# Performance work log

Hardware: AMD Instinct MI355X
Metric: run time of the kernel (lower is better)

Reference implementation:

```python
import jax, jax.numpy as jnp
import numpy as np

N = 30000      # nodes
E = 480000     # edges per relation (avg degree 16)
H = 4          # GAT heads
D = 64         # out_size per head
F1, F2 = 256, 128   # per-metapath input feature dims
SIN = 256      # sen_in_size
HD = H * D     # 256, semantic-attention in_size
OUT = 64       # final out_size


def _gat(feat, src, dst, W, al, ar, b):
    """DGL GATConv (eval mode, dropout=0), activation=relu6."""
    h = (feat @ W).reshape(N, H, D)                     # [N,H,D]
    el = (h * al).sum(-1)                               # [N,H]
    er = (h * ar).sum(-1)                               # [N,H]
    e = jax.nn.leaky_relu(el[src] + er[dst], 0.2)       # [E,H]
    m = jax.ops.segment_max(e, dst, N)                  # edge-softmax over incoming edges
    p = jnp.exp(e - m[dst])
    s = jax.ops.segment_sum(p, dst, N)
    a = p / s[dst]                                      # [E,H]
    out = jax.ops.segment_sum(a[:, :, None] * h[src], dst, N)  # [N,H,D]
    out = out + b.reshape(1, H, D)
    return jnp.clip(out, 0.0, 6.0).reshape(N, H * D)    # relu6, flatten(1)


def _gcn_layer(x, src, dst, W, b):
    """DGL GraphConv, norm='both': D_in^{-1/2} A D_out^{-1/2} X W (+ b)."""
    ones = jnp.ones(src.shape[0], x.dtype)
    deg_o = jnp.clip(jax.ops.segment_sum(ones, src, N), 1.0, None)
    deg_i = jnp.clip(jax.ops.segment_sum(ones, dst, N), 1.0, None)
    h = (x @ W) * (deg_o[:, None] ** -0.5)
    h = jax.ops.segment_sum(h[src], dst, N) * (deg_i[:, None] ** -0.5)
    return h if b is None else h + b


def setup_inputs():
    key = jax.random.key(0)
    ks = jax.random.split(key, 28)
    f32 = jnp.float32
    nrm = lambda k, shp: jax.random.normal(k, shp, f32) * 0.05
    ri = lambda k, shp: jax.random.randint(k, shp, 0, N, jnp.int32)
    return dict(
        feat0=jax.random.normal(ks[0], (N, F1), f32),
        feat1=jax.random.normal(ks[1], (N, F2), f32),
        sen_feat=jax.random.normal(ks[2], (N, SIN), f32),
        Wgat0=nrm(ks[11], (F1, H * D)), al0=nrm(ks[12], (H, D)), ar0=nrm(ks[13], (H, D)), b0=nrm(ks[14], (H * D,)),
        Wgat1=nrm(ks[15], (F2, H * D)), al1=nrm(ks[16], (H, D)), ar1=nrm(ks[17], (H, D)), b1=nrm(ks[18], (H * D,)),
        Wp1=nrm(ks[19], (HD, OUT)), bp1=nrm(ks[20], (OUT,)), wp2=nrm(ks[21], (OUT,)),
        Wf=nrm(ks[22], (HD, OUT)), bf=nrm(ks[23], (OUT,)),
        Wg1=nrm(ks[24], (SIN, OUT)), bg1=nrm(ks[25], (OUT,)), Wg2=nrm(ks[26], (OUT, OUT)),
        src0=ri(ks[3], (E,)), dst0=ri(ks[4], (E,)),
        src1=ri(ks[5], (E,)), dst1=ri(ks[6], (E,)),
        gsrc=ri(ks[7], (E,)), gdst=ri(ks[8], (E,)),
        asrc=ri(ks[9], (E,)), adst=ri(ks[10], (E,)),
        k=10,
    )


def reference(feat0, feat1, sen_feat,
              Wgat0, al0, ar0, b0, Wgat1, al1, ar1, b1,
              Wp1, bp1, wp2, Wf, bf, Wg1, bg1, Wg2,
              src0, dst0, src1, dst1, gsrc, gdst, asrc, adst, k):
    # per-metapath GAT embeddings
    z0 = _gat(feat0, src0, dst0, Wgat0, al0, ar0, b0)   # [N, HD]
    z1 = _gat(feat1, src1, dst1, Wgat1, al1, ar1, b1)   # [N, HD]
    z = jnp.stack([z0, z1], axis=1)                     # [N, M=2, HD]
    # PathAttention (semantic attention over metapaths)
    w = jnp.tanh(z @ Wp1 + bp1) @ wp2                   # [N, M]
    beta = jax.nn.softmax(w.mean(0))                    # [M]
    fused = jnp.einsum('m,nmf->nf', beta, z)            # [N, HD]
    Femb = fused @ Wf + bf                              # [N, OUT]
    # two-layer GCN on the sentence graph
    p1 = jnp.tanh(_gcn_layer(sen_feat, gsrc, gdst, Wg1, bg1))
    P = _gcn_layer(p1, gsrc, gdst, Wg2, None)           # [N, OUT]
    # spectral loss: fuse embeddings, trace of Laplacian quadratic form on first k dims
    Z = 0.5 * (Femb + P)                                # [N, OUT]
    Zk = Z[:, :k]
    diff = Zk[asrc] - Zk[adst]
    tr = 0.5 * jnp.sum(diff * diff)                     # tr(Zk^T (D - A) Zk)
    return (tr, Z)
```

## Files before the change

kernel.cpp:

```cpp
#include <hip/hip_runtime.h>
#include <math.h>

#define NN 30000
#define NE 480000
#define NBLK 118
#define NMT 235
#define NTRB 7500
#define CAPD 128

typedef unsigned short ushort_t;
typedef unsigned int uint_t;
typedef __attribute__((ext_vector_type(8))) short short8;
typedef __attribute__((ext_vector_type(4))) float f32x4;

__device__ __forceinline__ ushort_t f2bf(float x) {
  uint_t u = __float_as_uint(x);
  u = (u + 0x7FFF + ((u >> 16) & 1)) >> 16;
  return (ushort_t)u;
}
__device__ __forceinline__ float bf2f(ushort_t v) {
  return __uint_as_float(((uint_t)v) << 16);
}

__device__ __forceinline__ float wred(float v) {
#pragma unroll
  for (int off = 32; off > 0; off >>= 1) v += __shfl_xor(v, off);
  return v;
}

__global__ void prep_kernel(float4* __restrict__ zp, const float* __restrict__ W0,
                            const float* __restrict__ W1, const float* __restrict__ W2,
                            const float* __restrict__ W3, const float* __restrict__ W4,
                            ushort_t* __restrict__ T0, ushort_t* __restrict__ T1,
                            ushort_t* __restrict__ T2, ushort_t* __restrict__ T3,
                            ushort_t* __restrict__ T4, const float* __restrict__ F0,
                            const float* __restrict__ F1, ushort_t* __restrict__ B0,
                            ushort_t* __restrict__ B1) {
  int id = blockIdx.x * 256 + threadIdx.x;
  if (id < 52501) {
    zp[id] = make_float4(0.f, 0.f, 0.f, 0.f);
    return;
  }
  int wid = id - 52501;
  if (wid < 147456) {
    const float* W;
    ushort_t* T;
    int K, N, base;
    if (wid < 65536) { W = W0; T = T0; K = 256; N = 256; base = 0; }
    else if (wid < 98304) { W = W1; T = T1; K = 128; N = 256; base = 65536; }
    else if (wid < 114688) { W = W2; T = T2; K = 256; N = 64; base = 98304; }
    else if (wid < 131072) { W = W3; T = T3; K = 256; N = 64; base = 114688; }
    else { W = W4; T = T4; K = 256; N = 64; base = 131072; }
    int l = wid - base;
    int k = l / N, n = l - k * N;
    T[(size_t)n * K + k] = f2bf(W[l]);
    return;
  }
  int cid = wid - 147456;
  const float* S;
  ushort_t* D;
  if (cid < 960000) { S = F0; D = B0; }
  else {
    cid -= 960000;
    if (cid >= 480000) return;
    S = F1; D = B1;
  }
  const float4* p = (const float4*)(S + (size_t)cid * 8);
  float4 a = p[0], b = p[1];
  short8 o;
  o[0] = (short)f2bf(a.x); o[1] = (short)f2bf(a.y);
  o[2] = (short)f2bf(a.z); o[3] = (short)f2bf(a.w);
  o[4] = (short)f2bf(b.x); o[5] = (short)f2bf(b.y);
  o[6] = (short)f2bf(b.z); o[7] = (short)f2bf(b.w);
  *(short8*)(D + (size_t)cid * 8) = o;
}


__device__ __forceinline__ void mfma_core_f32(const float* __restrict__ A0,
                                              const ushort_t* __restrict__ BT, int K, int bm,
                                              short* __restrict__ As, short* __restrict__ Bs,
                                              f32x4 acc[2][4]) {
  int tid = threadIdx.x;
  int lane = tid & 63, w = tid >> 6;
  int q = lane >> 4, mr = lane & 15;
#pragma unroll 1
  for (int k0 = 0; k0 < K; k0 += 32) {
    {
      int r = tid >> 1, hf = tid & 1;
      int gr = bm + r;
      float4 f0 = make_float4(0.f, 0.f, 0.f, 0.f), f1 = f0, f2 = f0, f3 = f0;
      if (gr < NN) {
        const float4* pa = (const float4*)(A0 + (size_t)gr * K + k0 + hf * 16);
        f0 = pa[0]; f1 = pa[1]; f2 = pa[2]; f3 = pa[3];
      }
      short8 lo, hi;
      lo[0] = (short)f2bf(f0.x); lo[1] = (short)f2bf(f0.y);
      lo[2] = (short)f2bf(f0.z); lo[3] = (short)f2bf(f0.w);
      lo[4] = (short)f2bf(f1.x); lo[5] = (short)f2bf(f1.y);
      lo[6] = (short)f2bf(f1.z); lo[7] = (short)f2bf(f1.w);
      hi[0] = (short)f2bf(f2.x); hi[1] = (short)f2bf(f2.y);
      hi[2] = (short)f2bf(f2.z); hi[3] = (short)f2bf(f2.w);
      hi[4] = (short)f2bf(f3.x); hi[5] = (short)f2bf(f3.y);
      hi[6] = (short)f2bf(f3.z); hi[7] = (short)f2bf(f3.w);
      short* dst = As + r * 40 + hf * 16;
      *(short8*)(dst) = lo;
      *(short8*)(dst + 8) = hi;
    }
    {
      int n = tid >> 2, qk = tid & 3;
      short8 bv = *(const short8*)((const short*)BT + (size_t)n * K + k0 + qk * 8);
      *(short8*)(Bs + n * 40 + qk * 8) = bv;
    }
    __syncthreads();
    short8 a0 = *(short8*)(As + (w * 32 + mr) * 40 + q * 8);
    short8 a1 = *(short8*)(As + (w * 32 + 16 + mr) * 40 + q * 8);
#pragma unroll
    for (int j = 0; j < 4; ++j) {
      short8 b = *(short8*)(Bs + (j * 16 + mr) * 40 + q * 8);
      acc[0][j] = __builtin_amdgcn_mfma_f32_16x16x32_bf16(a0, b, acc[0][j], 0, 0, 0);
      acc[1][j] = __builtin_amdgcn_mfma_f32_16x16x32_bf16(a1, b, acc[1][j], 0, 0, 0);
    }
    __syncthreads();
  }
}

__device__ __forceinline__ void mfma_core2_bfK(const ushort_t* __restrict__ A0,
                                               const ushort_t* __restrict__ BT, int K, int bm,
                                               short* __restrict__ As, short* __restrict__ Bs,
                                               f32x4 acc[2][8]) {
  int tid = threadIdx.x;
  int lane = tid & 63, w = tid >> 6;
  int q = lane >> 4, mr = lane & 15;
#pragma unroll 1
  for (int k0 = 0; k0 < K; k0 += 32) {
    {
      int r = tid >> 1, hf = tid & 1;
      int gr = bm + r;
      short8 v0 = {0, 0, 0, 0, 0, 0, 0, 0}, v1 = v0;
      if (gr < NN) {
        const short* p0 = (const short*)A0 + (size_t)gr * K + k0 + hf * 16;
        v0 = *(const short8*)p0;
        v1 = *(const short8*)(p0 + 8);
      }
      short* dst = As + r * 40 + hf * 16;
      *(short8*)(dst) = v0;
      *(short8*)(dst + 8) = v1;
    }
    {
      int n = tid >> 1, qk = tid & 1;
      const short* src = (const short*)BT + (size_t)n * K + k0 + qk * 16;
      short8 b0 = *(const short8*)src;
      short8 b1 = *(const short8*)(src + 8);
      short* d = Bs + n * 40 + qk * 16;
      *(short8*)d = b0;
      *(short8*)(d + 8) = b1;
    }
    __syncthreads();
    short8 a0 = *(short8*)(As + (w * 32 + mr) * 40 + q * 8);
    short8 a1 = *(short8*)(As + (w * 32 + 16 + mr) * 40 + q * 8);
#pragma unroll
    for (int j = 0; j < 8; ++j) {
      short8 b = *(short8*)(Bs + (j * 16 + mr) * 40 + q * 8);
      acc[0][j] = __builtin_amdgcn_mfma_f32_16x16x32_bf16(a0, b, acc[0][j], 0, 0, 0);
      acc[1][j] = __builtin_amdgcn_mfma_f32_16x16x32_bf16(a1, b, acc[1][j], 0, 0, 0);
    }
    __syncthreads();
  }
}

__global__ __launch_bounds__(256) void mfma_all_kernel(
    const ushort_t* __restrict__ fB0, const ushort_t* __restrict__ fB1,
    const float* __restrict__ sen, const ushort_t* __restrict__ WT0,
    const ushort_t* __restrict__ WT1, const ushort_t* __restrict__ Wg1T,
    ushort_t* __restrict__ h0, ushort_t* __restrict__ h1, ushort_t* __restrict__ gcnA,
    const float* __restrict__ al0, const float* __restrict__ ar0, float* __restrict__ el0,
    float* __restrict__ er0, const float* __restrict__ al1, const float* __restrict__ ar1,
    float* __restrict__ el1, float* __restrict__ er1, const float* __restrict__ rdo) {
  __shared__ short As[128 * 40];
  __shared__ short Bs[128 * 40];
  int y = blockIdx.y;
  int bm = blockIdx.x * 128;
  int lane = threadIdx.x & 63, w = threadIdx.x >> 6;
  int q = lane >> 4, mr = lane & 15;
  if (y < 4) {
    int gsel = y >> 1, p = y & 1;
    const ushort_t* A = gsel ? fB1 : fB0;
    int K = gsel ? 128 : 256;
    const ushort_t* WT = gsel ? WT1 : WT0;
    ushort_t* H = gsel ? h1 : h0;
    const float* al = gsel ? al1 : al0;
    const float* ar = gsel ? ar1 : ar0;
    float* el = gsel ? el1 : el0;
    float* er = gsel ? er1 : er0;
    f32x4 acc[2][8];
#pragma unroll
    for (int i = 0; i < 2; ++i)
#pragma unroll
      for (int j = 0; j < 8; ++j) acc[i][j] = (f32x4){0.f, 0.f, 0.f, 0.f};
    mfma_core2_bfK(A, WT + (size_t)p * 128 * K, K, bm, As, Bs, acc);
    float alv[8], arv[8];
#pragma unroll
    for (int j = 0; j < 8; ++j) {
      alv[j] = al[p * 128 + j * 16 + mr];
      arv[j] = ar[p * 128 + j * 16 + mr];
    }
#pragma unroll
    for (int i = 0; i < 2; ++i)
#pragma unroll
      for (int r = 0; r < 4; ++r) {
        int gr = bm + w * 32 + i * 16 + q * 4 + r;
        float pl0 = 0.f, pr0 = 0.f, pl1 = 0.f, pr1 = 0.f;
#pragma unroll
        for (int j = 0; j < 4; ++j) {
          pl0 = fmaf(acc[i][j][r], alv[j], pl0);
          pr0 = fmaf(acc[i][j][r], arv[j], pr0);
          pl1 = fmaf(acc[i][j + 4][r], alv[j + 4], pl1);
          pr1 = fmaf(acc[i][j + 4][r], arv[j + 4], pr1);
        }
#pragma unroll
        for (int m = 1; m < 16; m <<= 1) {
          pl0 += __shfl_xor(pl0, m);
          pr0 += __shfl_xor(pr0, m);
          pl1 += __shfl_xor(pl1, m);
          pr1 += __shfl_xor(pr1, m);
        }
        if (gr < NN) {
          if (mr == 0) {
            el[gr * 4 + 2 * p] = pl0;
            er[gr * 4 + 2 * p] = pr0;
            el[gr * 4 + 2 * p + 1] = pl1;
            er[gr * 4 + 2 * p + 1] = pr1;
          }
#pragma unroll
          for (int j = 0; j < 8; ++j)
            H[(size_t)gr * 256 + p * 128 + j * 16 + mr] = f2bf(acc[i][j][r]);
        }
      }
  } else {
    f32x4 acc[2][4];
#pragma unroll
    for (int i = 0; i < 2; ++i)
#pragma unroll
      for (int j = 0; j < 4; ++j) acc[i][j] = (f32x4){0.f, 0.f, 0.f, 0.f};
    mfma_core_f32(sen, Wg1T, 256, bm, As, Bs, acc);
#pragma unroll
    for (int i = 0; i < 2; ++i)
#pragma unroll
      for (int r = 0; r < 4; ++r) {
        int gr = bm + w * 32 + i * 16 + q * 4 + r;
        if (gr < NN) {
          float sc = rdo[gr];
#pragma unroll
          for (int j = 0; j < 4; ++j)
            gcnA[(size_t)gr * 64 + j * 16 + mr] = f2bf(acc[i][j][r] * sc);
        }
      }
  }
}

__global__ __launch_bounds__(256) void mfma_attnwf_kernel(
    const ushort_t* __restrict__ z0, const ushort_t* __restrict__ z1,
    const ushort_t* __restrict__ WpfT, const float* __restrict__ bp1,
    const float* __restrict__ wp2, float* __restrict__ pbuf, ushort_t* __restrict__ Y0,
    ushort_t* __restrict__ Y1) {
  __shared__ short As[128 * 40];
  __shared__ short Bs[128 * 40];
  __shared__ float wsum[4];
  const ushort_t* A = blockIdx.y ? z1 : z0;
  ushort_t* Y = blockIdx.y ? Y1 : Y0;
  int bm = blockIdx.x * 128;
  f32x4 acc[2][8];
#pragma unroll
  for (int i = 0; i < 2; ++i)
#pragma unroll
    for (int j = 0; j < 8; ++j) acc[i][j] = (f32x4){0.f, 0.f, 0.f, 0.f};
  mfma_core2_bfK(A, WpfT, 256, bm, As, Bs, acc);
  int lane = threadIdx.x & 63, w = threadIdx.x >> 6;
  int q = lane >> 4, mr = lane & 15;
  float local = 0.f;
#pragma unroll
  for (int j = 0; j < 4; ++j) {
    int col = j * 16 + mr;
    float bp = bp1[col], wp = wp2[col];
#pragma unroll
    for (int i = 0; i < 2; ++i)
#pragma unroll
      for (int r = 0; r < 4; ++r) {
        int gr = bm + w * 32 + i * 16 + q * 4 + r;
        if (gr < NN) local += tanhf(acc[i][j][r] + bp) * wp;
      }
  }
  local = wred(local);
  if (lane == 0) wsum[w] = local;
#pragma unroll
  for (int j = 4; j < 8; ++j) {
    int col = (j - 4) * 16 + mr;
#pragma unroll
    for (int i = 0; i < 2; ++i)
#pragma unroll
      for (int r = 0; r < 4; ++r) {
        int gr = bm + w * 32 + i * 16 + q * 4 + r;
        if (gr < NN) Y[(size_t)gr * 64 + col] = f2bf(acc[i][j][r]);
      }
  }
  __syncthreads();
  if (threadIdx.x == 0)
    pbuf[blockIdx.y * NMT + blockIdx.x] = wsum[0] + wsum[1] + wsum[2] + wsum[3];
}

__global__ void hist_kernel(const int* __restrict__ d0, const int* __restrict__ d1,
                            const int* __restrict__ d2, const int* __restrict__ d3,
                            int* __restrict__ cnt) {
  int g = blockIdx.y;
  const int* d = g == 0 ? d0 : g == 1 ? d1 : g == 2 ? d2 : d3;
  int e = blockIdx.x * 256 + threadIdx.x;
  if (e < NE) atomicAdd(&cnt[g * NN + d[e]], 1);
}

__global__ __launch_bounds__(256) void scan_blocks_kernel(const int* __restrict__ cnt,
                                                          int* __restrict__ rows,
                                                          int* __restrict__ bsum) {
  __shared__ int sm[256];
  int g = blockIdx.y, t = threadIdx.x;
  int i = blockIdx.x * 256 + t;
  int v = (i < NN) ? cnt[g * NN + i] : 0;
  sm[t] = v;
  __syncthreads();
#pragma unroll
  for (int off = 1; off < 256; off <<= 1) {
    int tmp = (t >= off) ? sm[t - off] : 0;
    __syncthreads();
    sm[t] += tmp;
    __syncthreads();
  }
  if (i < NN) rows[g * (NN + 1) + i] = sm[t] - v;
  if (t == 255) bsum[g * NBLK + blockIdx.x] = sm[255];
}

__global__ __launch_bounds__(128) void scan_tops_kernel(int* __restrict__ bsum,
                                                        int* __restrict__ boff) {
  __shared__ int sm[128];
  int g = blockIdx.y, t = threadIdx.x;
  int v = (t < NBLK) ? bsum[g * NBLK + t] : 0;
  sm[t] = v;
  __syncthreads();
#pragma unroll
  for (int off = 1; off < 128; off <<= 1) {
    int tmp = (t >= off) ? sm[t - off] : 0;
    __syncthreads();
    sm[t] += tmp;
    __syncthreads();
  }
  if (t < NBLK) boff[g * NBLK + t] = sm[t] - v;
}

__global__ void add_off_kernel(int* __restrict__ rows, const int* __restrict__ boff) {
  int g = blockIdx.y, t = threadIdx.x;
  int i = blockIdx.x * 256 + t;
  if (i < NN) rows[g * (NN + 1) + i] += boff[g * NBLK + blockIdx.x];
  if (blockIdx.x == 0 && t == 0) rows[g * (NN + 1) + NN] = NE;
}

__global__ void scatter_kernel(const int* __restrict__ s0, const int* __restrict__ s1,
                               const int* __restrict__ s2, const int* __restrict__ d0,
                               const int* __restrict__ d1, const int* __restrict__ d2,
                               const int* __restrict__ rows, int* __restrict__ cnt2,
                               int* __restrict__ cols, const int* __restrict__ cnt_deg,
                               float* __restrict__ rdo, float* __restrict__ rdi,
                               const int* __restrict__ rows_g) {
  int g = blockIdx.y;
  if (g == 3) {
    int n = blockIdx.x * 256 + threadIdx.x;
    if (n < NN) {
      rdo[n] = rsqrtf(fmaxf((float)cnt_deg[n], 1.f));
      float di = (float)(rows_g[n + 1] - rows_g[n]);
      rdi[n] = rsqrtf(fmaxf(di, 1.f));
    }
    return;
  }
  const int* sp = g == 0 ? s0 : g == 1 ? s1 : s2;
  const int* dp = g == 0 ? d0 : g == 1 ? d1 : d2;
  int e = blockIdx.x * 256 + threadIdx.x;
  if (e >= NE) return;
  int d = dp[e];
  int pos = rows[g * (NN + 1) + d] + atomicAdd(&cnt2[g * NN + d], 1);
  cols[(size_t)g * NE + pos] = sp[e];
}

__global__ __launch_bounds__(256) void gat_node_kernel(
    const int* __restrict__ rows0, const int* __restrict__ cols0, const float* __restrict__ el0,
    const float* __restrict__ er0, const ushort_t* __restrict__ h0,
    const float* __restrict__ bias0, ushort_t* __restrict__ zz0, const int* __restrict__ rows1,
    const int* __restrict__ cols1, const float* __restrict__ el1, const float* __restrict__ er1,
    const ushort_t* __restrict__ h1, const float* __restrict__ bias1,
    ushort_t* __restrict__ zz1) {
  __shared__ float aw[4][CAPD][4];
  int g = blockIdx.y;
  const int* rows = g ? rows1 : rows0;
  const int* cols = g ? cols1 : cols0;
  const float* el = g ? el1 : el0;
  const float* er = g ? er1 : er0;
  const ushort_t* h = g ? h1 : h0;
  const float* bias = g ? bias1 : bias0;
  ushort_t* z = g ? zz1 : zz0;

  int lane = threadIdx.x & 63, w = threadIdx.x >> 6;
  int n = blockIdx.x * 4 + w;
  int r0 = rows[n], r1 = rows[n + 1];
  int deg = r1 - r0;
  float4 er4 = *(const float4*)&er[n * 4];
  float s0 = 0.f, s1 = 0.f, s2 = 0.f, s3 = 0.f;
  for (int j = lane; j < deg; j += 64) {
    int s = cols[r0 + j];
    float4 elv = *(const float4*)&el[s * 4];
    float v0 = elv.x + er4.x; v0 = v0 > 0.f ? v0 : 0.2f * v0;
    float v1 = elv.y + er4.y; v1 = v1 > 0.f ? v1 : 0.2f * v1;
    float v2 = elv.z + er4.z; v2 = v2 > 0.f ? v2 : 0.2f * v2;
    float v3 = elv.w + er4.w; v3 = v3 > 0.f ? v3 : 0.2f * v3;
    float e0 = __expf(v0), e1 = __expf(v1), e2 = __expf(v2), e3 = __expf(v3);
    s0 += e0; s1 += e1; s2 += e2; s3 += e3;
    if (j < CAPD) {
      aw[w][j][0] = e0; aw[w][j][1] = e1; aw[w][j][2] = e2; aw[w][j][3] = e3;
    }
  }
  s0 = wred(s0); s1 = wred(s1); s2 = wred(s2); s3 = wred(s3);
  __syncthreads();
  int hh = lane >> 4;
  float denom = hh == 0 ? s0 : hh == 1 ? s1 : hh == 2 ? s2 : s3;
  float myer = hh == 0 ? er4.x : hh == 1 ? er4.y : hh == 2 ? er4.z : er4.w;
  float invd = (deg > 0) ? 1.f / denom : 0.f;
  float4 acc = make_float4(0.f, 0.f, 0.f, 0.f);
  int jc = deg < CAPD ? deg : CAPD;
  for (int j = 0; j < jc; j += 16) {
    int si[16];
    float ai[16];
#pragma unroll
    for (int t = 0; t < 16; ++t) {
      int jj = j + t;
      int jx = jj < jc ? jj : jc - 1;
      si[t] = cols[r0 + jx];
      ai[t] = (jj < jc) ? aw[w][jj][hh] : 0.f;
    }
    ushort4 ui[16];
#pragma unroll
    for (int t = 0; t < 16; ++t) ui[t] = *(const ushort4*)&h[(size_t)si[t] * 256 + lane * 4];
#pragma unroll
    for (int t = 0; t < 16; ++t) {
      acc.x = fmaf(ai[t], bf2f(ui[t].x), acc.x);
      acc.y = fmaf(ai[t], bf2f(ui[t].y), acc.y);
      acc.z = fmaf(ai[t], bf2f(ui[t].z), acc.z);
      acc.w = fmaf(ai[t], bf2f(ui[t].w), acc.w);
    }
  }
  for (int j = jc; j < deg; ++j) {
    int s = cols[r0 + j];
    float v = el[s * 4 + hh] + myer;
    v = v > 0.f ? v : 0.2f * v;
    float a = __expf(v);
    ushort4 hu = *(const ushort4*)&h[(size_t)s * 256 + lane * 4];
    acc.x = fmaf(a, bf2f(hu.x), acc.x);
    acc.y = fmaf(a, bf2f(hu.y), acc.y);
    acc.z = fmaf(a, bf2f(hu.z), acc.z);
    acc.w = fmaf(a, bf2f(hu.w), acc.w);
  }
  float4 bv = *(const float4*)&bias[lane * 4];
  ushort4 o;
  o.x = f2bf(fminf(fmaxf(acc.x * invd + bv.x, 0.f), 6.f));
  o.y = f2bf(fminf(fmaxf(acc.y * invd + bv.y, 0.f), 6.f));
  o.z = f2bf(fminf(fmaxf(acc.z * invd + bv.z, 0.f), 6.f));
  o.w = f2bf(fminf(fmaxf(acc.w * invd + bv.w, 0.f), 6.f));
  *(ushort4*)&z[(size_t)n * 256 + lane * 4] = o;
}

__global__ __launch_bounds__(256) void gcn_gather12_kernel(
    const int* __restrict__ rows, const int* __restrict__ cols, const ushort_t* __restrict__ X,
    const float* __restrict__ rdi, const float* __restrict__ bg1, const float* __restrict__ Wg2,
    const float* __restrict__ rdo, ushort_t* __restrict__ out2, const float* __restrict__ pbuf,
    float* __restrict__ wb) {
  __shared__ float psm[4][64];
  int lane = threadIdx.x & 63, w = threadIdx.x >> 6;
  if (blockIdx.x == 0) {
    __shared__ float sm[8];
    int t = threadIdx.x;
    float a0 = 0.f, a1 = 0.f;
    for (int i = t; i < NMT; i += 256) {
      a0 += pbuf[i];
      a1 += pbuf[NMT + i];
    }
    a0 = wred(a0);
    a1 = wred(a1);
    if (lane == 0) { sm[w] = a0; sm[4 + w] = a1; }
    __syncthreads();
    if (t == 0) {
      float w0 = (sm[0] + sm[1] + sm[2] + sm[3]) * (1.0f / NN);
      float w1 = (sm[4] + sm[5] + sm[6] + sm[7]) * (1.0f / NN);
      float mx = fmaxf(w0, w1);
      float e0 = expf(w0 - mx), e1 = expf(w1 - mx);
      float inv = 1.f / (e0 + e1);
      wb[2] = e0 * inv;
      wb[3] = e1 * inv;
    }
  }
  int n = blockIdx.x * 4 + w;
  if (n >= NN) return;
  int r0 = rows[n], r1 = rows[n + 1];
  int eg = lane >> 4, fl = lane & 15;
  float facc[4] = {0.f, 0.f, 0.f, 0.f};
  for (int j = r0; j < r1; j += 16) {
    int si[4];
    float sel[4];
#pragma unroll
    for (int t = 0; t < 4; ++t) {
      int jj = j + 4 * t + eg;
      int jx = jj < r1 ? jj : r1 - 1;
      si[t] = cols[jx];
      sel[t] = (jj < r1) ? 1.f : 0.f;
    }
    ushort4 xv[4];
#pragma unroll
    for (int t = 0; t < 4; ++t) xv[t] = *(const ushort4*)&X[(size_t)si[t] * 64 + fl * 4];
#pragma unroll
    for (int t = 0; t < 4; ++t) {
      facc[0] = fmaf(sel[t], bf2f(xv[t].x), facc[0]);
      facc[1] = fmaf(sel[t], bf2f(xv[t].y), facc[1]);
      facc[2] = fmaf(sel[t], bf2f(xv[t].z), facc[2]);
      facc[3] = fmaf(sel[t], bf2f(xv[t].w), facc[3]);
    }
  }
#pragma unroll
  for (int u = 0; u < 4; ++u) {
    facc[u] += __shfl_xor(facc[u], 16);
    facc[u] += __shfl_xor(facc[u], 32);
  }
  if (eg == 0) *(float4*)&psm[w][fl * 4] = make_float4(facc[0], facc[1], facc[2], facc[3]);
  __syncthreads();
  float p = tanhf(psm[w][lane] * rdi[n] + bg1[lane]);
  float o = 0.f;
#pragma unroll
  for (int k = 0; k < 64; ++k) o = fmaf(__shfl(p, k), Wg2[k * 64 + lane], o);
  out2[(size_t)n * 64 + lane] = f2bf(o * rdo[n]);
}

__global__ __launch_bounds__(256) void gcn_gather2_kernel(
    const int* __restrict__ rows, const int* __restrict__ cols, const ushort_t* __restrict__ X,
    const float* __restrict__ rdi, const ushort_t* __restrict__ Y0,
    const ushort_t* __restrict__ Y1, const float* __restrict__ wb, const float* __restrict__ bf,
    const int* __restrict__ kptr, float* __restrict__ Zc, float* __restrict__ dout) {
  int lane = threadIdx.x & 63, w = threadIdx.x >> 6;
  int n = blockIdx.x * 4 + w;
  if (n >= NN) return;
  int r0 = rows[n], r1 = rows[n + 1];
  int eg = lane >> 4, fl = lane & 15;
  float facc[4] = {0.f, 0.f, 0.f, 0.f};
  for (int j = r0; j < r1; j += 16) {
    int si[4];
    float sel[4];
#pragma unroll
    for (int t = 0; t < 4; ++t) {
      int jj = j + 4 * t + eg;
      int jx = jj < r1 ? jj : r1 - 1;
      si[t] = cols[jx];
      sel[t] = (jj < r1) ? 1.f : 0.f;
    }
    ushort4 xv[4];
#pragma unroll
    for (int t = 0; t < 4; ++t) xv[t] = *(const ushort4*)&X[(size_t)si[t] * 64 + fl * 4];
#pragma unroll
    for (int t = 0; t < 4; ++t) {
      facc[0] = fmaf(sel[t], bf2f(xv[t].x), facc[0]);
      facc[1] = fmaf(sel[t], bf2f(xv[t].y), facc[1]);
      facc[2] = fmaf(sel[t], bf2f(xv[t].z), facc[2]);
      facc[3] = fmaf(sel[t], bf2f(xv[t].w), facc[3]);
    }
  }
#pragma unroll
  for (int u = 0; u < 4; ++u) {
    facc[u] += __shfl_xor(facc[u], 16);
    facc[u] += __shfl_xor(facc[u], 32);
  }
  if (eg == 0) {
    float ri = rdi[n];
    ushort4 y0 = *(const ushort4*)&Y0[(size_t)n * 64 + fl * 4];
    ushort4 y1 = *(const ushort4*)&Y1[(size_t)n * 64 + fl * 4];
    float4 bfv = *(const float4*)&bf[fl * 4];
    float w2 = wb[2], w3 = wb[3];
    float zv[4];
    zv[0] = 0.5f * (w2 * bf2f(y0.x) + w3 * bf2f(y1.x) + bfv.x + facc[0] * ri);
    zv[1] = 0.5f * (w2 * bf2f(y0.y) + w3 * bf2f(y1.y) + bfv.y + facc[1] * ri);
    zv[2] = 0.5f * (w2 * bf2f(y0.z) + w3 * bf2f(y1.z) + bfv.z + facc[2] * ri);
    zv[3] = 0.5f * (w2 * bf2f(y0.w) + w3 * bf2f(y1.w) + bfv.w + facc[3] * ri);
    float* dp = dout + 1 + (size_t)n * 64 + fl * 4;
    dp[0] = zv[0]; dp[1] = zv[1]; dp[2] = zv[2]; dp[3] = zv[3];
    int k = *kptr;
    if (fl < 4) {
      float4 zk;
      zk.x = (fl * 4 + 0 < k) ? zv[0] : 0.f;
      zk.y = (fl * 4 + 1 < k) ? zv[1] : 0.f;
      zk.z = (fl * 4 + 2 < k) ? zv[2] : 0.f;
      zk.w = (fl * 4 + 3 < k) ? zv[3] : 0.f;
      *(float4*)&Zc[(size_t)n * 16 + fl * 4] = zk;
    }
  }
}

__global__ __launch_bounds__(256) void tr_kernel(const int* __restrict__ asrc,
                                                 const int* __restrict__ adst,
                                                 const int* __restrict__ kptr,
                                                 const float* __restrict__ Zc,
                                                 const float* __restrict__ dout,
                                                 float* __restrict__ trbuf) {
  __shared__ float wsum[4];
  int lane = threadIdx.x & 63, w = threadIdx.x >> 6;
  int k = *kptr;
  int eg = lane >> 2, c0 = (lane & 3) * 4;
  int e = blockIdx.x * 64 + w * 16 + eg;
  float local = 0.f;
  if (e < NE) {
    int a = asrc[e], b = adst[e];
    if (k <= 16) {
      float4 za = *(const float4*)&Zc[(size_t)a * 16 + c0];
      float4 zb = *(const float4*)&Zc[(size_t)b * 16 + c0];
      float dx = za.x - zb.x, dy = za.y - zb.y, dz = za.z - zb.z, dw = za.w - zb.w;
      local = dx * dx + dy * dy + dz * dz + dw * dw;
    } else {
      const float* Za = dout + 1 + (size_t)a * 64;
      const float* Zb = dout + 1 + (size_t)b * 64;
#pragma unroll
      for (int st = 0; st < 4; ++st) {
#pragma unroll
        for (int t = 0; t < 4; ++t) {
          int c = c0 + st * 16 + t;
          if (c < k) {
            float d2 = Za[c] - Zb[c];
            local += d2 * d2;
          }
        }
      }
    }
  }
#pragma unroll
  for (int off = 32; off > 0; off >>= 1) local += __shfl_down(local, off);
  if (lane == 0) wsum[w] = local;
  __syncthreads();
  if (threadIdx.x == 0) trbuf[blockIdx.x] = wsum[0] + wsum[1] + wsum[2] + wsum[3];
}

__global__ __launch_bounds__(256) void tr_reduce_kernel(const float* __restrict__ trbuf,
                                                        float* __restrict__ dout) {
  __shared__ float sm[4];
  int t = threadIdx.x;
  float a = 0.f;
  for (int i = t; i < NTRB; i += 256) a += trbuf[i];
  a = wred(a);
  int lane = t & 63, w = t >> 6;
  if (lane == 0) sm[w] = a;
  __syncthreads();
  if (t == 0) dout[0] = 0.5f * (sm[0] + sm[1] + sm[2] + sm[3]);
}

extern "C" void kernel_launch(void* const* d_in, const int* in_sizes, int n_in, void* d_out,
                              int out_size, void* d_ws, size_t ws_size, hipStream_t stream) {
  const float* feat0 = (const float*)d_in[0];
  const float* feat1 = (const float*)d_in[1];
  const float* sen = (const float*)d_in[2];
  const float* Wgat0 = (const float*)d_in[3];
  const float* al0 = (const float*)d_in[4];
  const float* ar0 = (const float*)d_in[5];
  const float* b0 = (const float*)d_in[6];
  const float* Wgat1 = (const float*)d_in[7];
  const float* al1 = (const float*)d_in[8];
  const float* ar1 = (const float*)d_in[9];
  const float* b1 = (const float*)d_in[10];
  const float* Wp1 = (const float*)d_in[11];
  const float* bp1 = (const float*)d_in[12];
  const float* wp2 = (const float*)d_in[13];
  const float* Wf = (const float*)d_in[14];
  const float* bf = (const float*)d_in[15];
  const float* Wg1 = (const float*)d_in[16];
  const float* bg1 = (const float*)d_in[17];
  const float* Wg2 = (const float*)d_in[18];
  const int* src0 = (const int*)d_in[19];
  const int* dst0 = (const int*)d_in[20];
  const int* src1 = (const int*)d_in[21];
  const int* dst1 = (const int*)d_in[22];
  const int* gsrc = (const int*)d_in[23];
  const int* gdst = (const int*)d_in[24];
  const int* asrc = (const int*)d_in[25];
  const int* adst = (const int*)d_in[26];
  const int* kptr = (const int*)d_in[27];
  float* out = (float*)d_out;
  float* ws = (float*)d_ws;

  float* wb = ws;
  int* cnt = (int*)(ws + 4);
  int* cnt2 = (int*)(ws + 120004);
  float* rdo = ws + 210004;
  float* rdi = ws + 240004;
  int* rows = (int*)(ws + 270004);
  int* bsum = (int*)(ws + 360008);
  int* boff = (int*)(ws + 360364);
  int* cols = (int*)(ws + 360720);
  float* el0 = ws + 1800720;
  float* er0 = ws + 1920720;
  float* el1 = ws + 2040720;
  float* er1 = ws + 2160720;
  float* pbuf = ws + 2280720;
  float* trbuf = el0;
  ushort_t* h0 = (ushort_t*)(ws + 2283068);
  ushort_t* h1 = (ushort_t*)(ws + 6123068);
  ushort_t* z0 = (ushort_t*)(ws + 9963068);
  ushort_t* z1 = (ushort_t*)(ws + 13803068);
  ushort_t* gcnA = (ushort_t*)(ws + 17643068);
  ushort_t* gcnA2 = (ushort_t*)(ws + 18603068);
  ushort_t* Y0 = (ushort_t*)(ws + 19563068);
  ushort_t* Y1 = (ushort_t*)(ws + 20523068);
  ushort_t* WT0 = (ushort_t*)(ws + 21483068);
  ushort_t* WT1 = (ushort_t*)(ws + 21515836);
  ushort_t* WpfT = (ushort_t*)(ws + 21532220);
  ushort_t* Wg1T = (ushort_t*)(ws + 21548604);
  float* Zc = ws + 21556796;

  int* rows_g = rows + 2 * (NN + 1);
  int* cols_g = cols + 2 * NE;
  int* cnt_deg = cnt + 3 * NN;

  ushort_t* fB0 = z0;
  ushort_t* fB1 = z1;

  prep_kernel<<<6407, 256, 0, stream>>>((float4*)ws, Wgat0, Wgat1, Wp1, Wf, Wg1, WT0, WT1, WpfT,
                                        WpfT + 16384, Wg1T, feat0, feat1, fB0, fB1);

  hist_kernel<<<dim3(1875, 4), 256, 0, stream>>>(dst0, dst1, gdst, gsrc, cnt);
  scan_blocks_kernel<<<dim3(NBLK, 3), 256, 0, stream>>>(cnt, rows, bsum);
  scan_tops_kernel<<<dim3(1, 3), 128, 0, stream>>>(bsum, boff);
  add_off_kernel<<<dim3(NBLK, 3), 256, 0, stream>>>(rows, boff);
  scatter_kernel<<<dim3(1875, 4), 256, 0, stream>>>(src0, src1, gsrc, dst0, dst1, gdst, rows,
                                                    cnt2, cols, cnt_deg, rdo, rdi, rows_g);

  mfma_all_kernel<<<dim3(NMT, 5), 256, 0, stream>>>(fB0, fB1, sen, WT0, WT1, Wg1T, h0, h1,
                                                    gcnA, al0, ar0, el0, er0, al1, ar1, el1,
                                                    er1, rdo);

  gat_node_kernel<<<dim3(7500, 2), 256, 0, stream>>>(rows, cols, el0, er0, h0, b0, z0,
                                                     rows + (NN + 1), cols + NE, el1, er1, h1,
                                                     b1, z1);

  mfma_attnwf_kernel<<<dim3(NMT, 2), 256, 0, stream>>>(z0, z1, WpfT, bp1, wp2, pbuf, Y0, Y1);

  gcn_gather12_kernel<<<7500, 256, 0, stream>>>(rows_g, cols_g, gcnA, rdi, bg1, Wg2, rdo, gcnA2,
                                                pbuf, wb);
  gcn_gather2_kernel<<<7500, 256, 0, stream>>>(rows_g, cols_g, gcnA2, rdi, Y0, Y1, wb, bf, kptr,
                                               Zc, out);

  tr_kernel<<<NTRB, 256, 0, stream>>>(asrc, adst, kptr, Zc, out, trbuf);
  tr_reduce_kernel<<<1, 256, 0, stream>>>(trbuf, out);
}
```

Baseline: 515.7 us.

## Merge GAT aggregation and first GCN gather into one launch; inline beta softmax

The GAT node aggregation for both metapaths and the first GCN gather-plus-Wg2 layer become one kernel launch with 22500 blocks. Block index ranges pick which branch runs, so the independent GCN work can fill the GPU alongside the GAT gathers. The semantic-attention softmax that used to be done by block 0 of the GCN kernel and written to wb is now recomputed per wave inside gcn_gather2 from pbuf. This removes a launch and a global round-trip, at the cost of every wave re-reducing 2x235 partial sums.

```diff
diff --git a/kernel.cpp b/kernel.cpp
--- a/kernel.cpp
+++ b/kernel.cpp
@@ -387,120 +387,158 @@
   cols[(size_t)g * NE + pos] = sp[e];
 }
 
-__global__ __launch_bounds__(256) void gat_node_kernel(
+__global__ __launch_bounds__(256) void gat_g12_kernel(
     const int* __restrict__ rows0, const int* __restrict__ cols0, const float* __restrict__ el0,
     const float* __restrict__ er0, const ushort_t* __restrict__ h0,
     const float* __restrict__ bias0, ushort_t* __restrict__ zz0, const int* __restrict__ rows1,
     const int* __restrict__ cols1, const float* __restrict__ el1, const float* __restrict__ er1,
     const ushort_t* __restrict__ h1, const float* __restrict__ bias1,
-    ushort_t* __restrict__ zz1) {
+    ushort_t* __restrict__ zz1, const int* __restrict__ rows_g, const int* __restrict__ cols_g,
+    const ushort_t* __restrict__ X, const float* __restrict__ rdi,
+    const float* __restrict__ bg1, const float* __restrict__ Wg2,
+    const float* __restrict__ rdo, ushort_t* __restrict__ out2) {
   __shared__ float aw[4][CAPD][4];
-  int g = blockIdx.y;
-  const int* rows = g ? rows1 : rows0;
-  const int* cols = g ? cols1 : cols0;
-  const float* el = g ? el1 : el0;
-  const float* er = g ? er1 : er0;
-  const ushort_t* h = g ? h1 : h0;
-  const float* bias = g ? bias1 : bias0;
-  ushort_t* z = g ? zz1 : zz0;
-
   int lane = threadIdx.x & 63, w = threadIdx.x >> 6;
-  int n = blockIdx.x * 4 + w;
-  int r0 = rows[n], r1 = rows[n + 1];
-  int deg = r1 - r0;
-  float4 er4 = *(const float4*)&er[n * 4];
-  float s0 = 0.f, s1 = 0.f, s2 = 0.f, s3 = 0.f;
-  for (int j = lane; j < deg; j += 64) {
-    int s = cols[r0 + j];
-    float4 elv = *(const float4*)&el[s * 4];
-    float v0 = elv.x + er4.x; v0 = v0 > 0.f ? v0 : 0.2f * v0;
-    float v1 = elv.y + er4.y; v1 = v1 > 0.f ? v1 : 0.2f * v1;
-    float v2 = elv.z + er4.z; v2 = v2 > 0.f ? v2 : 0.2f * v2;
-    float v3 = elv.w + er4.w; v3 = v3 > 0.f ? v3 : 0.2f * v3;
-    float e0 = __expf(v0), e1 = __expf(v1), e2 = __expf(v2), e3 = __expf(v3);
-    s0 += e0; s1 += e1; s2 += e2; s3 += e3;
-    if (j < CAPD) {
-      aw[w][j][0] = e0; aw[w][j][1] = e1; aw[w][j][2] = e2; aw[w][j][3] = e3;
-    }
-  }
-  s0 = wred(s0); s1 = wred(s1); s2 = wred(s2); s3 = wred(s3);
-  __syncthreads();
-  int hh = lane >> 4;
-  float denom = hh == 0 ? s0 : hh == 1 ? s1 : hh == 2 ? s2 : s3;
-  float myer = hh == 0 ? er4.x : hh == 1 ? er4.y : hh == 2 ? er4.z : er4.w;
-  float invd = (deg > 0) ? 1.f / denom : 0.f;
-  float4 acc = make_float4(0.f, 0.f, 0.f, 0.f);
-  int jc = deg < CAPD ? deg : CAPD;
-  for (int j = 0; j < jc; j += 16) {
-    int si[16];
-    float ai[16];
-#pragma unroll
-    for (int t = 0; t < 16; ++t) {
-      int jj = j + t;
-      int jx = jj < jc ? jj : jc - 1;
-      si[t] = cols[r0 + jx];
-      ai[t] = (jj < jc) ? aw[w][jj][hh] : 0.f;
-    }
-    ushort4 ui[16];
-#pragma unroll
-    for (int t = 0; t < 16; ++t) ui[t] = *(const ushort4*)&h[(size_t)si[t] * 256 + lane * 4];
-#pragma unroll
-    for (int t = 0; t < 16; ++t) {
-      acc.x = fmaf(ai[t], bf2f(ui[t].x), acc.x);
-      acc.y = fmaf(ai[t], bf2f(ui[t].y), acc.y);
-      acc.z = fmaf(ai[t], bf2f(ui[t].z), acc.z);
-      acc.w = fmaf(ai[t], bf2f(ui[t].w), acc.w);
-    }
-  }
-  for (int j = jc; j < deg; ++j) {
-    int s = cols[r0 + j];
-    float v = el[s * 4 + hh] + myer;
-    v = v > 0.f ? v : 0.2f * v;
-    float a = __expf(v);
-    ushort4 hu = *(const ushort4*)&h[(size_t)s * 256 + lane * 4];
-    acc.x = fmaf(a, bf2f(hu.x), acc.x);
-    acc.y = fmaf(a, bf2f(hu.y), acc.y);
-    acc.z = fmaf(a, bf2f(hu.z), acc.z);
-    acc.w = fmaf(a, bf2f(hu.w), acc.w);
-  }
-  float4 bv = *(const float4*)&bias[lane * 4];
-  ushort4 o;
-  o.x = f2bf(fminf(fmaxf(acc.x * invd + bv.x, 0.f), 6.f));
-  o.y = f2bf(fminf(fmaxf(acc.y * invd + bv.y, 0.f), 6.f));
-  o.z = f2bf(fminf(fmaxf(acc.z * invd + bv.z, 0.f), 6.f));
-  o.w = f2bf(fminf(fmaxf(acc.w * invd + bv.w, 0.f), 6.f));
-  *(ushort4*)&z[(size_t)n * 256 + lane * 4] = o;
-}
-
-__global__ __launch_bounds__(256) void gcn_gather12_kernel(
+  int bx = blockIdx.x;
+  if (bx < 15000) {
+    int g = bx >= 7500;
+    int bl = g ? bx - 7500 : bx;
+    const int* rows = g ? rows1 : rows0;
+    const int* cols = g ? cols1 : cols0;
+    const float* el = g ? el1 : el0;
+    const float* er = g ? er1 : er0;
+    const ushort_t* h = g ? h1 : h0;
+    const float* bias = g ? bias1 : bias0;
+    ushort_t* z = g ? zz1 : zz0;
+
+    int n = bl * 4 + w;
+    int r0 = rows[n], r1 = rows[n + 1];
+    int deg = r1 - r0;
+    float4 er4 = *(const float4*)&er[n * 4];
+    float s0 = 0.f, s1 = 0.f, s2 = 0.f, s3 = 0.f;
+    for (int j = lane; j < deg; j += 64) {
+      int s = cols[r0 + j];
+      float4 elv = *(const float4*)&el[s * 4];
+      float v0 = elv.x + er4.x; v0 = v0 > 0.f ? v0 : 0.2f * v0;
+      float v1 = elv.y + er4.y; v1 = v1 > 0.f ? v1 : 0.2f * v1;
+      float v2 = elv.z + er4.z; v2 = v2 > 0.f ? v2 : 0.2f * v2;
+      float v3 = elv.w + er4.w; v3 = v3 > 0.f ? v3 : 0.2f * v3;
+      float e0 = __expf(v0), e1 = __expf(v1), e2 = __expf(v2), e3 = __expf(v3);
+      s0 += e0; s1 += e1; s2 += e2; s3 += e3;
+      if (j < CAPD) {
+        aw[w][j][0] = e0; aw[w][j][1] = e1; aw[w][j][2] = e2; aw[w][j][3] = e3;
+      }
+    }
+    s0 = wred(s0); s1 = wred(s1); s2 = wred(s2); s3 = wred(s3);
+    __syncthreads();
+    int hh = lane >> 4;
+    float denom = hh == 0 ? s0 : hh == 1 ? s1 : hh == 2 ? s2 : s3;
+    float myer = hh == 0 ? er4.x : hh == 1 ? er4.y : hh == 2 ? er4.z : er4.w;
+    float invd = (deg > 0) ? 1.f / denom : 0.f;
+    float4 acc = make_float4(0.f, 0.f, 0.f, 0.f);
+    int jc = deg < CAPD ? deg : CAPD;
+    for (int j = 0; j < jc; j += 16) {
+      int si[16];
+      float ai[16];
+#pragma unroll
+      for (int t = 0; t < 16; ++t) {
+        int jj = j + t;
+        int jx = jj < jc ? jj : jc - 1;
+        si[t] = cols[r0 + jx];
+        ai[t] = (jj < jc) ? aw[w][jj][hh] : 0.f;
+      }
+      ushort4 ui[16];
+#pragma unroll
+      for (int t = 0; t < 16; ++t) ui[t] = *(const ushort4*)&h[(size_t)si[t] * 256 + lane * 4];
+#pragma unroll
+      for (int t = 0; t < 16; ++t) {
+        acc.x = fmaf(ai[t], bf2f(ui[t].x), acc.x);
+        acc.y = fmaf(ai[t], bf2f(ui[t].y), acc.y);
+        acc.z = fmaf(ai[t], bf2f(ui[t].z), acc.z);
+        acc.w = fmaf(ai[t], bf2f(ui[t].w), acc.w);
+      }
+    }
+    for (int j = jc; j < deg; ++j) {
+      int s = cols[r0 + j];
+      float v = el[s * 4 + hh] + myer;
+      v = v > 0.f ? v : 0.2f * v;
+      float a = __expf(v);
+      ushort4 hu = *(const ushort4*)&h[(size_t)s * 256 + lane * 4];
+      acc.x = fmaf(a, bf2f(hu.x), acc.x);
+      acc.y = fmaf(a, bf2f(hu.y), acc.y);
+      acc.z = fmaf(a, bf2f(hu.z), acc.z);
+      acc.w = fmaf(a, bf2f(hu.w), acc.w);
+    }
+    float4 bv = *(const float4*)&bias[lane * 4];
+    ushort4 o;
+    o.x = f2bf(fminf(fmaxf(acc.x * invd + bv.x, 0.f), 6.f));
+    o.y = f2bf(fminf(fmaxf(acc.y * invd + bv.y, 0.f), 6.f));
+    o.z = f2bf(fminf(fmaxf(acc.z * invd + bv.z, 0.f), 6.f));
+    o.w = f2bf(fminf(fmaxf(acc.w * invd + bv.w, 0.f), 6.f));
+    *(ushort4*)&z[(size_t)n * 256 + lane * 4] = o;
+  } else {
+    float(*psm)[64] = (float(*)[64])aw;
+    int n = (bx - 15000) * 4 + w;
+    if (n >= NN) return;
+    int r0 = rows_g[n], r1 = rows_g[n + 1];
+    int eg = lane >> 4, fl = lane & 15;
+    float facc[4] = {0.f, 0.f, 0.f, 0.f};
+    for (int j = r0; j < r1; j += 16) {
+      int si[4];
+      float sel[4];
+#pragma unroll
+      for (int t = 0; t < 4; ++t) {
+        int jj = j + 4 * t + eg;
+        int jx = jj < r1 ? jj : r1 - 1;
+        si[t] = cols_g[jx];
+        sel[t] = (jj < r1) ? 1.f : 0.f;
+      }
+      ushort4 xv[4];
+#pragma unroll
+      for (int t = 0; t < 4; ++t) xv[t] = *(const ushort4*)&X[(size_t)si[t] * 64 + fl * 4];
+#pragma unroll
+      for (int t = 0; t < 4; ++t) {
+        facc[0] = fmaf(sel[t], bf2f(xv[t].x), facc[0]);
+        facc[1] = fmaf(sel[t], bf2f(xv[t].y), facc[1]);
+        facc[2] = fmaf(sel[t], bf2f(xv[t].z), facc[2]);
+        facc[3] = fmaf(sel[t], bf2f(xv[t].w), facc[3]);
+      }
+    }
+#pragma unroll
+    for (int u = 0; u < 4; ++u) {
+      facc[u] += __shfl_xor(facc[u], 16);
+      facc[u] += __shfl_xor(facc[u], 32);
+    }
+    if (eg == 0) *(float4*)&psm[w][fl * 4] = make_float4(facc[0], facc[1], facc[2], facc[3]);
+    __syncthreads();
+    float p = tanhf(psm[w][lane] * rdi[n] + bg1[lane]);
+    float o = 0.f;
+#pragma unroll
+    for (int k = 0; k < 64; ++k) o = fmaf(__shfl(p, k), Wg2[k * 64 + lane], o);
+    out2[(size_t)n * 64 + lane] = f2bf(o * rdo[n]);
+  }
+}
+
+__global__ __launch_bounds__(256) void gcn_gather2_kernel(
     const int* __restrict__ rows, const int* __restrict__ cols, const ushort_t* __restrict__ X,
-    const float* __restrict__ rdi, const float* __restrict__ bg1, const float* __restrict__ Wg2,
-    const float* __restrict__ rdo, ushort_t* __restrict__ out2, const float* __restrict__ pbuf,
-    float* __restrict__ wb) {
-  __shared__ float psm[4][64];
+    const float* __restrict__ rdi, const ushort_t* __restrict__ Y0,
+    const ushort_t* __restrict__ Y1, const float* __restrict__ pbuf,
+    const float* __restrict__ bf, const int* __restrict__ kptr, float* __restrict__ Zc,
+    float* __restrict__ dout) {
   int lane = threadIdx.x & 63, w = threadIdx.x >> 6;
-  if (blockIdx.x == 0) {
-    __shared__ float sm[8];
-    int t = threadIdx.x;
-    float a0 = 0.f, a1 = 0.f;
-    for (int i = t; i < NMT; i += 256) {
-      a0 += pbuf[i];
-      a1 += pbuf[NMT + i];
-    }
-    a0 = wred(a0);
-    a1 = wred(a1);
-    if (lane == 0) { sm[w] = a0; sm[4 + w] = a1; }
-    __syncthreads();
-    if (t == 0) {
-      float w0 = (sm[0] + sm[1] + sm[2] + sm[3]) * (1.0f / NN);
-      float w1 = (sm[4] + sm[5] + sm[6] + sm[7]) * (1.0f / NN);
-      float mx = fmaxf(w0, w1);
-      float e0 = expf(w0 - mx), e1 = expf(w1 - mx);
-      float inv = 1.f / (e0 + e1);
-      wb[2] = e0 * inv;
-      wb[3] = e1 * inv;
-    }
-  }
+  float b0a = 0.f, b1a = 0.f;
+  for (int i = lane; i < NMT; i += 64) {
+    b0a += pbuf[i];
+    b1a += pbuf[NMT + i];
+  }
+  b0a = wred(b0a);
+  b1a = wred(b1a);
+  float w0 = b0a * (1.0f / NN), w1 = b1a * (1.0f / NN);
+  float mx = fmaxf(w0, w1);
+  float be0 = __expf(w0 - mx), be1 = __expf(w1 - mx);
+  float binv = 1.f / (be0 + be1);
+  float wb2 = be0 * binv, wb3 = be1 * binv;
+
   int n = blockIdx.x * 4 + w;
   if (n >= NN) return;
   int r0 = rows[n], r1 = rows[n + 1];
@@ -532,63 +570,16 @@
     facc[u] += __shfl_xor(facc[u], 16);
     facc[u] += __shfl_xor(facc[u], 32);
   }
-  if (eg == 0) *(float4*)&psm[w][fl * 4] = make_float4(facc[0], facc[1], facc[2], facc[3]);
-  __syncthreads();
-  float p = tanhf(psm[w][lane] * rdi[n] + bg1[lane]);
-  float o = 0.f;
-#pragma unroll
-  for (int k = 0; k < 64; ++k) o = fmaf(__shfl(p, k), Wg2[k * 64 + lane], o);
-  out2[(size_t)n * 64 + lane] = f2bf(o * rdo[n]);
-}
-
-__global__ __launch_bounds__(256) void gcn_gather2_kernel(
-    const int* __restrict__ rows, const int* __restrict__ cols, const ushort_t* __restrict__ X,
-    const float* __restrict__ rdi, const ushort_t* __restrict__ Y0,
-    const ushort_t* __restrict__ Y1, const float* __restrict__ wb, const float* __restrict__ bf,
-    const int* __restrict__ kptr, float* __restrict__ Zc, float* __restrict__ dout) {
-  int lane = threadIdx.x & 63, w = threadIdx.x >> 6;
-  int n = blockIdx.x * 4 + w;
-  if (n >= NN) return;
-  int r0 = rows[n], r1 = rows[n + 1];
-  int eg = lane >> 4, fl = lane & 15;
-  float facc[4] = {0.f, 0.f, 0.f, 0.f};
-  for (int j = r0; j < r1; j += 16) {
-    int si[4];
-    float sel[4];
-#pragma unroll
-    for (int t = 0; t < 4; ++t) {
-      int jj = j + 4 * t + eg;
-      int jx = jj < r1 ? jj : r1 - 1;
-      si[t] = cols[jx];
-      sel[t] = (jj < r1) ? 1.f : 0.f;
-    }
-    ushort4 xv[4];
-#pragma unroll
-    for (int t = 0; t < 4; ++t) xv[t] = *(const ushort4*)&X[(size_t)si[t] * 64 + fl * 4];
-#pragma unroll
-    for (int t = 0; t < 4; ++t) {
-      facc[0] = fmaf(sel[t], bf2f(xv[t].x), facc[0]);
-      facc[1] = fmaf(sel[t], bf2f(xv[t].y), facc[1]);
-      facc[2] = fmaf(sel[t], bf2f(xv[t].z), facc[2]);
-      facc[3] = fmaf(sel[t], bf2f(xv[t].w), facc[3]);
-    }
-  }
-#pragma unroll
-  for (int u = 0; u < 4; ++u) {
-    facc[u] += __shfl_xor(facc[u], 16);
-    facc[u] += __shfl_xor(facc[u], 32);
-  }
   if (eg == 0) {
     float ri = rdi[n];
     ushort4 y0 = *(const ushort4*)&Y0[(size_t)n * 64 + fl * 4];
     ushort4 y1 = *(const ushort4*)&Y1[(size_t)n * 64 + fl * 4];
     float4 bfv = *(const float4*)&bf[fl * 4];
-    float w2 = wb[2], w3 = wb[3];
     float zv[4];
-    zv[0] = 0.5f * (w2 * bf2f(y0.x) + w3 * bf2f(y1.x) + bfv.x + facc[0] * ri);
-    zv[1] = 0.5f * (w2 * bf2f(y0.y) + w3 * bf2f(y1.y) + bfv.y + facc[1] * ri);
-    zv[2] = 0.5f * (w2 * bf2f(y0.z) + w3 * bf2f(y1.z) + bfv.z + facc[2] * ri);
-    zv[3] = 0.5f * (w2 * bf2f(y0.w) + w3 * bf2f(y1.w) + bfv.w + facc[3] * ri);
+    zv[0] = 0.5f * (wb2 * bf2f(y0.x) + wb3 * bf2f(y1.x) + bfv.x + facc[0] * ri);
+    zv[1] = 0.5f * (wb2 * bf2f(y0.y) + wb3 * bf2f(y1.y) + bfv.y + facc[1] * ri);
+    zv[2] = 0.5f * (wb2 * bf2f(y0.z) + wb3 * bf2f(y1.z) + bfv.z + facc[2] * ri);
+    zv[3] = 0.5f * (wb2 * bf2f(y0.w) + wb3 * bf2f(y1.w) + bfv.w + facc[3] * ri);
     float* dp = dout + 1 + (size_t)n * 64 + fl * 4;
     dp[0] = zv[0]; dp[1] = zv[1]; dp[2] = zv[2]; dp[3] = zv[3];
     int k = *kptr;
@@ -723,6 +714,7 @@
   int* rows_g = rows + 2 * (NN + 1);
   int* cols_g = cols + 2 * NE;
   int* cnt_deg = cnt + 3 * NN;
+  (void)wb;
 
   ushort_t* fB0 = z0;
   ushort_t* fB1 = z1;
@@ -741,16 +733,14 @@
                                                     gcnA, al0, ar0, el0, er0, al1, ar1, el1,
                                                     er1, rdo);
 
-  gat_node_kernel<<<dim3(7500, 2), 256, 0, stream>>>(rows, cols, el0, er0, h0, b0, z0,
-                                                     rows + (NN + 1), cols + NE, el1, er1, h1,
-                                                     b1, z1);
+  gat_g12_kernel<<<22500, 256, 0, stream>>>(rows, cols, el0, er0, h0, b0, z0,
+                                            rows + (NN + 1), cols + NE, el1, er1, h1, b1, z1,
+                                            rows_g, cols_g, gcnA, rdi, bg1, Wg2, rdo, gcnA2);
 
   mfma_attnwf_kernel<<<dim3(NMT, 2), 256, 0, stream>>>(z0, z1, WpfT, bp1, wp2, pbuf, Y0, Y1);
 
-  gcn_gather12_kernel<<<7500, 256, 0, stream>>>(rows_g, cols_g, gcnA, rdi, bg1, Wg2, rdo, gcnA2,
-                                                pbuf, wb);
-  gcn_gather2_kernel<<<7500, 256, 0, stream>>>(rows_g, cols_g, gcnA2, rdi, Y0, Y1, wb, bf, kptr,
-                                               Zc, out);
+  gcn_gather2_kernel<<<7500, 256, 0, stream>>>(rows_g, cols_g, gcnA2, rdi, Y0, Y1, pbuf, bf,
+                                               kptr, Zc, out);
 
   tr_kernel<<<NTRB, 256, 0, stream>>>(asrc, adst, kptr, Zc, out, trbuf);
   tr_reduce_kernel<<<1, 256, 0, stream>>>(trbuf, out);
```

New measurement: 520.6 us. No clear change (+1.0%).
